# Kernel tuning notes

Measured on AMD Instinct MI355X. Metric: run time of the kernel, lower is better.

Reference implementation:

```python
import jax, jax.numpy as jnp
import numpy as np

B, T, P, D = 32, 8, 196, 768
M = 10
NUM_CLASSES = 100
NUM_IDX = 98
P_MASK = 0.5


def setup_inputs() -> dict:
    key = jax.random.key(0)
    ks = jax.random.split(key, 16)
    s = 0.02
    inp = {
        'visual': jax.random.normal(ks[0], (B, T * P, D), jnp.float32),
        'audio': jax.random.normal(ks[1], (B, D), jnp.float32),
        'causal': jax.random.normal(ks[2], (B, M, D), jnp.float32),
        'random_mask': jax.random.uniform(ks[3], (B, T, P, D)) < P_MASK,
        'Wa': jax.random.normal(ks[4], (D, D), jnp.float32) * s,
        'ba': jnp.zeros((D,), jnp.float32),
        'Wv': jax.random.normal(ks[5], (D, D), jnp.float32) * s,
        'bv': jnp.zeros((D,), jnp.float32),
        'Waa': jax.random.normal(ks[6], (D, D), jnp.float32) * s,
        'baa': jnp.zeros((D,), jnp.float32),
        'Wav': jax.random.normal(ks[7], (D, D), jnp.float32) * s,
        'bav': jnp.zeros((D,), jnp.float32),
        'Wf': jax.random.normal(ks[8], (D, D), jnp.float32) * s,
        'bf': jnp.zeros((D,), jnp.float32),
        'Wf2': jax.random.normal(ks[9], (D, 1), jnp.float32) * s,
        'bf2': jnp.zeros((1,), jnp.float32),
        'Wc': jax.random.normal(ks[10], (D, NUM_CLASSES), jnp.float32) * s,
        'bc': jnp.zeros((NUM_CLASSES,), jnp.float32),
        'causal_param': jnp.zeros((1,), jnp.float32),
    }
    return inp


def reference(visual, audio, causal, random_mask, Wa, ba, Wv, bv, Waa, baa,
              Wav, bav, Wf, bf, Wf2, bf2, Wc, bc, causal_param):
    vis = visual.reshape(visual.shape[0], T, -1, D)  # [B,8,196,768]

    # causal_intervention_mean_feature4
    cp = jax.nn.sigmoid(causal_param)                 # soft_clamp2, [1]
    feats = causal @ Wf + bf                          # [B,M,D]
    feats2 = jnp.swapaxes(causal @ Wf2 + bf2, 1, 2)   # [B,1,M]
    fw = jax.nn.softmax(jnp.tanh(feats), axis=1)      # [B,M,D]
    ci = jnp.einsum('bom,bmd->bd', feats2, fw * causal)  # bmm + squeeze
    audio2 = cp * ci + audio                          # [B,D]

    # audio_visual_attention1
    pa = jnp.tanh(audio2 @ Waa + baa)                 # [B,D]
    pv = jnp.tanh(vis @ Wav + bav)                    # [B,T,P,D]
    sscore = pv * pa[:, None, None, :]                # einsum ijkd,id->ijkd
    sattn = jax.nn.softmax(sscore, axis=2)            # softmax over patches
    patch = jnp.sum(sattn, axis=-1)                   # [B,T,P]
    thresh = jnp.sort(patch, axis=-1)[:, :, NUM_IDX]  # per (b,t) threshold
    spa_mask = patch < thresh[:, :, None]             # [B,T,P]
    final_mask = ~(spa_mask[..., None] & random_mask) # [B,T,P,D]
    sfilt = jnp.where(final_mask, sattn, 0.0)

    sav = jnp.sum(sfilt * pv, axis=2)                 # [B,T,D]
    tattn = jax.nn.softmax(sav * pa[:, None, :], axis=1)

    vp = jnp.sum(sfilt * vis, axis=2)                 # [B,T,D]
    vp = jnp.sum(tattn * vp, axis=1)                  # [B,D]

    af = jax.nn.relu(audio2 @ Wa + ba)
    vf = jax.nn.relu(vp @ Wv + bv)
    logits = (af + vf) @ Wc + bc                      # [B,num_classes]
    return logits
```

## Files before the change

kernel.cpp:

```cpp
#include <hip/hip_runtime.h>
#include <hip/hip_bf16.h>
#include <hip/hip_fp16.h>
#include <math.h>

#define BB 32
#define TT 8
#define PP 196
#define DD 768
#define MM 10
#define NCLS 100
#define NIDX 98

typedef __attribute__((ext_vector_type(8))) short short8v;
typedef __attribute__((ext_vector_type(4))) float float4v;

__device__ __forceinline__ float fast_tanh(float x) {
    float e = __expf(2.0f * x);
    return 1.0f - 2.0f / (e + 1.0f);
}
__device__ __forceinline__ unsigned short f2bf(float x) {
    __hip_bfloat16 h = __float2bfloat16(x);
    return *(unsigned short*)&h;
}
__device__ __forceinline__ float bf2f(unsigned short h) {
    return __uint_as_float(((unsigned)h) << 16);
}
__device__ __forceinline__ unsigned short f2h(float x) {
    __half h = __float2half(x);
    return *(unsigned short*)&h;
}
__device__ __forceinline__ float h2f(unsigned short u) {
    __half h = *(__half*)&u;
    return __half2float(h);
}

__global__ __launch_bounds__(256) void k_prep(
    const float* __restrict__ vis, unsigned short* __restrict__ visb,
    const unsigned int* __restrict__ rm, int* __restrict__ mode) {
    const size_t NC = (size_t)BB * TT * PP * DD / 8;
    size_t gid = (size_t)blockIdx.x * 256 + threadIdx.x;
    size_t nthr = (size_t)gridDim.x * 256;
    for (size_t i = gid; i < NC; i += nthr) {
        const float4* s = (const float4*)(vis + i * 8);
        float4 x = s[0], y = s[1];
        __hip_bfloat162 h;
        unsigned int u0, u1, u2, u3;
        h = __float22bfloat162_rn(make_float2(x.x, x.y)); u0 = *(unsigned int*)&h;
        h = __float22bfloat162_rn(make_float2(x.z, x.w)); u1 = *(unsigned int*)&h;
        h = __float22bfloat162_rn(make_float2(y.x, y.y)); u2 = *(unsigned int*)&h;
        h = __float22bfloat162_rn(make_float2(y.z, y.w)); u3 = *(unsigned int*)&h;
        uint4 o; o.x = u0; o.y = u1; o.z = u2; o.w = u3;
        ((uint4*)visb)[i] = o;
    }
    if (blockIdx.x == 0) {
        __shared__ int f_ni, f_nf;
        if (threadIdx.x == 0) { f_ni = 0; f_nf = 0; }
        __syncthreads();
        int ni = 0, nf = 0;
        for (int i = threadIdx.x; i < 16384; i += 256) {
            unsigned int v = rm[i];
            ni |= (v > 1u) ? 1 : 0;
            nf |= (v != 0u && v != 0x3F800000u) ? 1 : 0;
        }
        if (ni) atomicOr(&f_ni, 1);
        if (nf) atomicOr(&f_nf, 1);
        __syncthreads();
        if (threadIdx.x == 0) *mode = f_ni ? (f_nf ? 2 : 1) : 0;
    }
}

__global__ __launch_bounds__(256) void k_split_w(const float* __restrict__ W,
    unsigned short* __restrict__ ht) {
    __shared__ float tile[32][33];
    int bn = blockIdx.x * 32;
    int bk = blockIdx.y * 32;
    int tx = threadIdx.x & 31, ty = threadIdx.x >> 5;
    #pragma unroll
    for (int i = 0; i < 4; ++i)
        tile[ty + i * 8][tx] = W[(size_t)(bk + ty + i * 8) * DD + bn + tx];
    __syncthreads();
    #pragma unroll
    for (int i = 0; i < 4; ++i) {
        int n = bn + ty + i * 8, k = bk + tx;
        ht[(size_t)n * DD + k] = f2bf(tile[tx][ty + i * 8]);
    }
}

__global__ __launch_bounds__(768) void k_feats_partial(
    const float* __restrict__ causal, const float* __restrict__ Wf,
    const float* __restrict__ Wf2,
    float* __restrict__ pf, float* __restrict__ pf2) {
    int b = blockIdx.x, kc = blockIdx.y;
    int k0 = kc * 256;
    int t = threadIdx.x;
    __shared__ float cs[MM][256];
    __shared__ float red[MM][12];
    for (int i = t; i < MM * 256; i += 768)
        cs[i >> 8][i & 255] = causal[((size_t)b * MM + (i >> 8)) * DD + k0 + (i & 255)];
    __syncthreads();
    int wave = t >> 6, lane = t & 63;
    float w2v = (t < 256) ? Wf2[k0 + t] : 0.f;
    #pragma unroll
    for (int m = 0; m < MM; ++m) {
        float p = (t < 256) ? cs[m][t] * w2v : 0.f;
        #pragma unroll
        for (int o = 32; o > 0; o >>= 1) p += __shfl_down(p, o);
        if (lane == 0) red[m][wave] = p;
    }
    __syncthreads();
    if (t < MM) {
        float s = 0.f;
        #pragma unroll
        for (int wv = 0; wv < 4; ++wv) s += red[t][wv];
        pf2[(b * 3 + kc) * MM + t] = s;
    }
    float acc[MM];
    #pragma unroll
    for (int m = 0; m < MM; ++m) acc[m] = 0.f;
    #pragma unroll 4
    for (int k = 0; k < 256; ++k) {
        float wv = Wf[(size_t)(k0 + k) * DD + t];
        #pragma unroll
        for (int m = 0; m < MM; ++m) acc[m] = fmaf(cs[m][k], wv, acc[m]);
    }
    #pragma unroll
    for (int m = 0; m < MM; ++m)
        pf[(((size_t)b * 3 + kc) * MM + m) * DD + t] = acc[m];
}

__global__ __launch_bounds__(768) void k_audio2a(
    const float* __restrict__ causal, const float* __restrict__ audio,
    const float* __restrict__ pf, const float* __restrict__ pf2,
    const float* __restrict__ bf, const float* __restrict__ bf2,
    const float* __restrict__ cparam, float* __restrict__ a2) {
    int b = blockIdx.x;
    int t = threadIdx.x;
    float cp = 1.0f / (1.0f + __expf(-cparam[0]));
    float tf[MM], f2[MM];
    float mx = -1e30f;
    #pragma unroll
    for (int m = 0; m < MM; ++m) {
        float acc = bf[t];
        float s2 = bf2[0];
        #pragma unroll
        for (int kc = 0; kc < 3; ++kc) {
            acc += pf[(((size_t)b * 3 + kc) * MM + m) * DD + t];
            s2 += pf2[(b * 3 + kc) * MM + m];
        }
        tf[m] = fast_tanh(acc);
        f2[m] = s2;
        mx = fmaxf(mx, tf[m]);
    }
    float s = 0.f;
    #pragma unroll
    for (int m = 0; m < MM; ++m) { tf[m] = __expf(tf[m] - mx); s += tf[m]; }
    float inv = 1.0f / s;
    float ci = 0.f;
    #pragma unroll
    for (int m = 0; m < MM; ++m)
        ci += f2[m] * (tf[m] * inv) * causal[((size_t)b * MM + m) * DD + t];
    a2[(size_t)b * DD + t] = cp * ci + audio[(size_t)b * DD + t];
}

__global__ __launch_bounds__(256) void k_audio2b(
    const float* __restrict__ a2,
    const float* __restrict__ Waa, const float* __restrict__ baa,
    const float* __restrict__ Wa, const float* __restrict__ ba,
    float* __restrict__ pa, float* __restrict__ af, float* __restrict__ colsum) {
    int gid0 = (blockIdx.y * 24 + blockIdx.x) * 256 + threadIdx.x;
    for (int i = gid0; i < BB * TT * DD; i += 48 * 256) colsum[i] = 0.f;
    __shared__ float a2s[16][DD + 4];
    int sel = blockIdx.y;
    const float* W = sel ? Wa : Waa;
    int t = threadIdx.x;
    int c = blockIdx.x * 32 + (t & 31);
    int slot = t >> 5;
    float bias = sel ? ba[c] : baa[c];
    #pragma unroll
    for (int g = 0; g < 2; ++g) {
        if (g) __syncthreads();
        for (int i = t; i < 16 * DD; i += 256)
            a2s[i / DD][i % DD] = a2[(size_t)(g * 16 + i / DD) * DD + i % DD];
        __syncthreads();
        float acc0 = 0.f, acc1 = 0.f;
        #pragma unroll 8
        for (int k = 0; k < DD; ++k) {
            float wv = W[(size_t)k * DD + c];
            acc0 = fmaf(a2s[slot][k], wv, acc0);
            acc1 = fmaf(a2s[slot + 8][k], wv, acc1);
        }
        int b0 = g * 16 + slot, b1 = b0 + 8;
        if (sel == 0) {
            pa[(size_t)b0 * DD + c] = fast_tanh(acc0 + bias);
            pa[(size_t)b1 * DD + c] = fast_tanh(acc1 + bias);
        } else {
            af[(size_t)b0 * DD + c] = fmaxf(acc0 + bias, 0.f);
            af[(size_t)b1 * DD + c] = fmaxf(acc1 + bias, 0.f);
        }
    }
}

__global__ __launch_bounds__(256, 5) void k_pv_mfma(
    const unsigned short* __restrict__ visb, const unsigned short* __restrict__ Wht,
    const float* __restrict__ bav, const float* __restrict__ pa,
    unsigned short* __restrict__ pvh, float* __restrict__ colsum)
{
    __shared__ unsigned short As[128 * 64];
    __shared__ unsigned short Bs[128 * 64];
    int wg = blockIdx.x;
    int lin = (wg & 7) * 294 + (wg >> 3);
    int mt = lin / 6, nt = lin % 6;
    int i0 = mt * 128, n0 = nt * 128;
    int t = threadIdx.x, w = t >> 6, l = t & 63;
    int wm = (w >> 1) * 64, wn = (w & 1) * 64;

    float4v zero4 = {0.f, 0.f, 0.f, 0.f};
    float4v acc[4][4];
    #pragma unroll
    for (int a = 0; a < 4; ++a)
        #pragma unroll
        for (int b = 0; b < 4; ++b) acc[a][b] = zero4;

    int brow[4], bcs[4];
    #pragma unroll
    for (int j = 0; j < 4; ++j) {
        int row = (w * 4 + j) * 8 + (l >> 3);
        brow[j] = row;
        bcs[j] = (l & 7) ^ (row & 7);
    }

    for (int wnd = 0; wnd < 12; ++wnd) {
        __syncthreads();
        int kw = wnd * 64;
        #pragma unroll
        for (int j = 0; j < 4; ++j) {
            size_t aoff = (size_t)(i0 + brow[j]) * DD + kw + bcs[j] * 8;
            __builtin_amdgcn_global_load_lds(
                (const __attribute__((address_space(1))) unsigned int*)(visb + aoff),
                (__attribute__((address_space(3))) unsigned int*)&As[(w * 4 + j) * 512],
                16, 0, 0);
            size_t boff = (size_t)(n0 + brow[j]) * DD + kw + bcs[j] * 8;
            __builtin_amdgcn_global_load_lds(
                (const __attribute__((address_space(1))) unsigned int*)(Wht + boff),
                (__attribute__((address_space(3))) unsigned int*)&Bs[(w * 4 + j) * 512],
                16, 0, 0);
        }
        __syncthreads();
        #pragma unroll
        for (int kk = 0; kk < 2; ++kk) {
            short8v ahf[4], bhf[4];
            #pragma unroll
            for (int mr = 0; mr < 4; ++mr) {
                int row = wm + mr * 16 + (l & 15);
                int c = kk * 4 + (l >> 4);
                ahf[mr] = *(const short8v*)&As[row * 64 + ((c ^ (row & 7)) * 8)];
            }
            #pragma unroll
            for (int nc = 0; nc < 4; ++nc) {
                int row = wn + nc * 16 + (l & 15);
                int c = kk * 4 + (l >> 4);
                bhf[nc] = *(const short8v*)&Bs[row * 64 + ((c ^ (row & 7)) * 8)];
            }
            #pragma unroll
            for (int mr = 0; mr < 4; ++mr)
                #pragma unroll
                for (int nc = 0; nc < 4; ++nc)
                    acc[mr][nc] = __builtin_amdgcn_mfma_f32_16x16x32_bf16(
                        ahf[mr], bhf[nc], acc[mr][nc], 0, 0, 0);
        }
    }
    float* cred = (float*)&As[0];
    __syncthreads();
    if (t < 256) cred[t] = 0.f;
    __syncthreads();
    int bt0 = i0 / PP;
    int btbound = (bt0 + 1) * PP;
    #pragma unroll
    for (int nc = 0; nc < 4; ++nc) {
        int cl = wn + nc * 16 + (l & 15);
        int col = n0 + cl;
        float bias = bav[col];
        #pragma unroll
        for (int mr = 0; mr < 4; ++mr) {
            int row0 = i0 + wm + mr * 16 + ((l >> 4) << 2);
            int bq = row0 / (TT * PP);
            float pav = pa[(size_t)bq * DD + col];
            float esum = 0.f;
            #pragma unroll
            for (int v = 0; v < 4; ++v) {
                unsigned short pb = f2h(fast_tanh(acc[mr][nc][v] + bias));
                pvh[(size_t)(row0 + v) * DD + col] = pb;
                esum += __expf(h2f(pb) * pav);
            }
            int btg = (row0 >= btbound) ? 1 : 0;
            atomicAdd(&cred[btg * 128 + cl], esum);
        }
    }
    __syncthreads();
    if (t < 256) {
        int btg = t >> 7, cl = t & 127;
        if (btg == 0 || btbound < i0 + 128)
            atomicAdd(&colsum[(size_t)(bt0 + btg) * DD + n0 + cl], cred[t]);
    }
}

__global__ __launch_bounds__(768) void k_patch(
    const unsigned short* __restrict__ pvh, const float* __restrict__ pa,
    const float* __restrict__ colsum, unsigned char* __restrict__ spa_g) {
    int bt = blockIdx.x;
    int b = bt >> 3;
    size_t base = (size_t)bt * PP * DD;
    __shared__ float2 pi[DD];
    __shared__ float patch[PP];
    int t = threadIdx.x;
    float pav = pa[(size_t)b * DD + t];
    float inv = 1.0f / colsum[(size_t)bt * DD + t];
    pi[t] = make_float2(pav, inv);
    __syncthreads();
    int wave = t >> 6, lane = t & 63;
    for (int p = wave; p < PP; p += 12) {
        const uint2* rv = (const uint2*)(pvh + base + (size_t)p * DD);
        float sum = 0.f;
        #pragma unroll
        for (int j = lane; j < 192; j += 64) {
            uint2 v = rv[j];
            int c = j * 4;
            float2 q0 = pi[c], q1 = pi[c + 1], q2 = pi[c + 2], q3 = pi[c + 3];
            sum += __expf(h2f((unsigned short)(v.x & 0xFFFFu)) * q0.x) * q0.y
                 + __expf(h2f((unsigned short)(v.x >> 16)) * q1.x) * q1.y
                 + __expf(h2f((unsigned short)(v.y & 0xFFFFu)) * q2.x) * q2.y
                 + __expf(h2f((unsigned short)(v.y >> 16)) * q3.x) * q3.y;
        }
        #pragma unroll
        for (int o = 32; o > 0; o >>= 1) sum += __shfl_down(sum, o);
        if (lane == 0) patch[p] = sum;
    }
    __syncthreads();
    if (t < PP) {
        float x = patch[t];
        int c = 0;
        for (int q = 0; q < PP; ++q) c += (patch[q] <= x) ? 1 : 0;
        spa_g[bt * PP + t] = (c <= NIDX) ? 1 : 0;
    }
}

__global__ __launch_bounds__(768) void k_masked(
    const unsigned short* __restrict__ pvh, const unsigned short* __restrict__ visb,
    const void* __restrict__ rmask, const int* __restrict__ mode_p,
    const float* __restrict__ pa, const float* __restrict__ colsum,
    const unsigned char* __restrict__ spa_g,
    float* __restrict__ sav, float* __restrict__ vpt) {
    int bt = blockIdx.x;
    int half = blockIdx.y;
    int b = bt >> 3;
    size_t base = (size_t)bt * PP * DD;
    __shared__ unsigned char spa[PP];
    __shared__ float red_s[2][384];
    __shared__ float red_v[2][384];
    int t = threadIdx.x;
    if (t < PP) spa[t] = spa_g[bt * PP + t];
    int pg = (t >= 384) ? 1 : 0;
    int c = t - pg * 384;
    int col = half * 384 + c;
    int p0 = pg * 98, p1 = p0 + 98;
    float pav = pa[(size_t)b * DD + col];
    float inv = 1.0f / colsum[(size_t)bt * DD + col];
    __syncthreads();
    const unsigned short* pvb = pvh + base + col;
    const unsigned short* vib = visb + base + col;
    float sava = 0.f, vpa = 0.f;
    int mode = *mode_p;
    if (mode == 0) {
        const int* mb = (const int*)rmask + base + col;
        #pragma unroll 7
        for (int p = p0; p < p1; ++p) {
            float pvv = h2f(pvb[(size_t)p * DD]);
            float sa = __expf(pvv * pav) * inv;
            bool km = !(spa[p] && (mb[(size_t)p * DD] != 0));
            if (km) { sava = fmaf(sa, pvv, sava); vpa = fmaf(sa, bf2f(vib[(size_t)p * DD]), vpa); }
        }
    } else if (mode == 1) {
        const float* mb = (const float*)rmask + base + col;
        #pragma unroll 7
        for (int p = p0; p < p1; ++p) {
            float pvv = h2f(pvb[(size_t)p * DD]);
            float sa = __expf(pvv * pav) * inv;
            bool km = !(spa[p] && (mb[(size_t)p * DD] != 0.f));
            if (km) { sava = fmaf(sa, pvv, sava); vpa = fmaf(sa, bf2f(vib[(size_t)p * DD]), vpa); }
        }
    } else {
        const unsigned char* mb = (const unsigned char*)rmask + base + col;
        #pragma unroll 7
        for (int p = p0; p < p1; ++p) {
            float pvv = h2f(pvb[(size_t)p * DD]);
            float sa = __expf(pvv * pav) * inv;
            bool km = !(spa[p] && (mb[(size_t)p * DD] != 0));
            if (km) { sava = fmaf(sa, pvv, sava); vpa = fmaf(sa, bf2f(vib[(size_t)p * DD]), vpa); }
        }
    }
    red_s[pg][c] = sava;
    red_v[pg][c] = vpa;
    __syncthreads();
    if (t < 384) {
        int col2 = half * 384 + t;
        sav[(size_t)bt * DD + col2] = red_s[0][t] + red_s[1][t];
        vpt[(size_t)bt * DD + col2] = red_v[0][t] + red_v[1][t];
    }
}

__global__ __launch_bounds__(768) void k_tail_a(
    const float* __restrict__ sav, const float* __restrict__ vpt,
    const float* __restrict__ pa, float* __restrict__ vp) {
    int b = blockIdx.x;
    int t = threadIdx.x;
    float pav = pa[(size_t)b * DD + t];
    float x[TT];
    float mx = -1e30f;
    #pragma unroll
    for (int k = 0; k < TT; ++k) {
        x[k] = sav[((size_t)b * TT + k) * DD + t] * pav;
        mx = fmaxf(mx, x[k]);
    }
    float s = 0.f;
    #pragma unroll
    for (int k = 0; k < TT; ++k) { x[k] = __expf(x[k] - mx); s += x[k]; }
    float inv = 1.0f / s;
    float acc = 0.f;
    #pragma unroll
    for (int k = 0; k < TT; ++k)
        acc += x[k] * inv * vpt[((size_t)b * TT + k) * DD + t];
    vp[(size_t)b * DD + t] = acc;
}

__global__ __launch_bounds__(256) void k_tail_b(
    const float* __restrict__ vp, const float* __restrict__ af,
    const float* __restrict__ Wv, const float* __restrict__ bv,
    float* __restrict__ h) {
    __shared__ float vs[16][DD + 4];
    int t = threadIdx.x;
    int c = blockIdx.x * 32 + (t & 31);
    int slot = t >> 5;
    float bias = bv[c];
    #pragma unroll
    for (int g = 0; g < 2; ++g) {
        if (g) __syncthreads();
        for (int i = t; i < 16 * DD; i += 256)
            vs[i / DD][i % DD] = vp[(size_t)(g * 16 + i / DD) * DD + i % DD];
        __syncthreads();
        float acc0 = 0.f, acc1 = 0.f;
        #pragma unroll 8
        for (int k = 0; k < DD; ++k) {
            float wv = Wv[(size_t)k * DD + c];
            acc0 = fmaf(vs[slot][k], wv, acc0);
            acc1 = fmaf(vs[slot + 8][k], wv, acc1);
        }
        int b0 = g * 16 + slot, b1 = b0 + 8;
        h[(size_t)b0 * DD + c] = fmaxf(acc0 + bias, 0.f) + af[(size_t)b0 * DD + c];
        h[(size_t)b1 * DD + c] = fmaxf(acc1 + bias, 0.f) + af[(size_t)b1 * DD + c];
    }
}

__global__ __launch_bounds__(256) void k_tail_c(
    const float* __restrict__ h, const float* __restrict__ Wc,
    const float* __restrict__ bc, float* __restrict__ out) {
    int t = threadIdx.x;
    int c = blockIdx.x * 8 + (t & 7);
    int b = t >> 3;
    if (c >= NCLS) return;
    float acc = bc[c];
    #pragma unroll 8
    for (int k = 0; k < DD; ++k)
        acc = fmaf(h[(size_t)b * DD + k], Wc[(size_t)k * NCLS + c], acc);
    out[(size_t)b * NCLS + c] = acc;
}

extern "C" void kernel_launch(void* const* d_in, const int* in_sizes, int n_in,
                              void* d_out, int out_size, void* d_ws, size_t ws_size,
                              hipStream_t stream) {
    const float* visual = (const float*)d_in[0];
    const float* audio  = (const float*)d_in[1];
    const float* causal = (const float*)d_in[2];
    const void*  rmask  = d_in[3];
    const float* Wa   = (const float*)d_in[4];
    const float* ba   = (const float*)d_in[5];
    const float* Wv   = (const float*)d_in[6];
    const float* bv   = (const float*)d_in[7];
    const float* Waa  = (const float*)d_in[8];
    const float* baa  = (const float*)d_in[9];
    const float* Wav  = (const float*)d_in[10];
    const float* bav  = (const float*)d_in[11];
    const float* Wf   = (const float*)d_in[12];
    const float* bf   = (const float*)d_in[13];
    const float* Wf2  = (const float*)d_in[14];
    const float* bf2  = (const float*)d_in[15];
    const float* Wc   = (const float*)d_in[16];
    const float* bc   = (const float*)d_in[17];
    const float* cpar = (const float*)d_in[18];
    float* out = (float*)d_out;

    const size_t NE = (size_t)BB * TT * PP * DD;
    unsigned short* Wht = (unsigned short*)d_ws;
    float* pfreg = (float*)(Wht + (size_t)DD * DD);
    float* colsum = pfreg;
    float* savw  = colsum + (size_t)BB * TT * DD;
    float* vptw  = savw + (size_t)BB * TT * DD;
    float* vpw   = vptw + (size_t)BB * TT * DD;
    float* hw    = vpw + (size_t)BB * DD;
    unsigned char* spa_g = (unsigned char*)(hw + (size_t)BB * DD);
    float* pf    = pfreg;
    float* pf2   = pfreg + (size_t)BB * 3 * MM * DD;
    float* a2w   = pf2 + 1024;
    float* paw   = a2w + (size_t)BB * DD;
    float* afw   = paw + (size_t)BB * DD;
    int*   modew = (int*)(afw + (size_t)BB * DD);
    unsigned short* visb = (unsigned short*)(modew + 16);
    unsigned short* pvh  = visb + NE;

    k_prep<<<2048, 256, 0, stream>>>(visual, visb, (const unsigned int*)rmask, modew);
    k_split_w<<<dim3(24, 24), 256, 0, stream>>>(Wav, Wht);
    k_feats_partial<<<dim3(BB, 3), 768, 0, stream>>>(causal, Wf, Wf2, pf, pf2);
    k_audio2a<<<BB, 768, 0, stream>>>(causal, audio, pf, pf2, bf, bf2, cpar, a2w);
    k_audio2b<<<dim3(24, 2), 256, 0, stream>>>(a2w, Waa, baa, Wa, ba, paw, afw, colsum);
    k_pv_mfma<<<2352, 256, 0, stream>>>(visb, Wht, bav, paw, pvh, colsum);
    k_patch<<<BB * TT, 768, 0, stream>>>(pvh, paw, colsum, spa_g);
    k_masked<<<dim3(BB * TT, 2), 768, 0, stream>>>(pvh, visb, rmask, modew, paw,
                                                   colsum, spa_g, savw, vptw);
    k_tail_a<<<BB, 768, 0, stream>>>(savw, vptw, paw, vpw);
    k_tail_b<<<24, 256, 0, stream>>>(vpw, afw, Wv, bv, hw);
    k_tail_c<<<13, 256, 0, stream>>>(hw, Wc, bc, out);
}
```

Baseline: 532.7 us.

## Merge prep kernels, double-buffer GEMM LDS, and stage pv output through LDS

Folds the bf16 conversion, weight transpose and feats-partial kernels into one launch that dispatches on block index, removing two kernel launches. The pv MFMA GEMM now double-buffers its A/B tiles in LDS so the next K-window's global->LDS loads overlap the current MFMAs, with one barrier per iteration. The fp16 pv tile is first written to swizzled LDS and then stored to global memory as coalesced 16-byte rows. The price is twice the LDS per block, which lowers the occupancy hint from 5 to 2 blocks per CU and may hurt latency hiding.

```diff
diff --git a/kernel.cpp b/kernel.cpp
--- a/kernel.cpp
+++ b/kernel.cpp
@@ -34,98 +34,103 @@
     return __half2float(h);
 }
 
-__global__ __launch_bounds__(256) void k_prep(
+__global__ __launch_bounds__(768) void k_prep_all(
     const float* __restrict__ vis, unsigned short* __restrict__ visb,
-    const unsigned int* __restrict__ rm, int* __restrict__ mode) {
-    const size_t NC = (size_t)BB * TT * PP * DD / 8;
-    size_t gid = (size_t)blockIdx.x * 256 + threadIdx.x;
-    size_t nthr = (size_t)gridDim.x * 256;
-    for (size_t i = gid; i < NC; i += nthr) {
-        const float4* s = (const float4*)(vis + i * 8);
-        float4 x = s[0], y = s[1];
-        __hip_bfloat162 h;
-        unsigned int u0, u1, u2, u3;
-        h = __float22bfloat162_rn(make_float2(x.x, x.y)); u0 = *(unsigned int*)&h;
-        h = __float22bfloat162_rn(make_float2(x.z, x.w)); u1 = *(unsigned int*)&h;
-        h = __float22bfloat162_rn(make_float2(y.x, y.y)); u2 = *(unsigned int*)&h;
-        h = __float22bfloat162_rn(make_float2(y.z, y.w)); u3 = *(unsigned int*)&h;
-        uint4 o; o.x = u0; o.y = u1; o.z = u2; o.w = u3;
-        ((uint4*)visb)[i] = o;
-    }
-    if (blockIdx.x == 0) {
-        __shared__ int f_ni, f_nf;
-        if (threadIdx.x == 0) { f_ni = 0; f_nf = 0; }
-        __syncthreads();
-        int ni = 0, nf = 0;
-        for (int i = threadIdx.x; i < 16384; i += 256) {
-            unsigned int v = rm[i];
-            ni |= (v > 1u) ? 1 : 0;
-            nf |= (v != 0u && v != 0x3F800000u) ? 1 : 0;
-        }
-        if (ni) atomicOr(&f_ni, 1);
-        if (nf) atomicOr(&f_nf, 1);
-        __syncthreads();
-        if (threadIdx.x == 0) *mode = f_ni ? (f_nf ? 2 : 1) : 0;
-    }
-}
-
-__global__ __launch_bounds__(256) void k_split_w(const float* __restrict__ W,
-    unsigned short* __restrict__ ht) {
-    __shared__ float tile[32][33];
-    int bn = blockIdx.x * 32;
-    int bk = blockIdx.y * 32;
-    int tx = threadIdx.x & 31, ty = threadIdx.x >> 5;
-    #pragma unroll
-    for (int i = 0; i < 4; ++i)
-        tile[ty + i * 8][tx] = W[(size_t)(bk + ty + i * 8) * DD + bn + tx];
-    __syncthreads();
-    #pragma unroll
-    for (int i = 0; i < 4; ++i) {
-        int n = bn + ty + i * 8, k = bk + tx;
-        ht[(size_t)n * DD + k] = f2bf(tile[tx][ty + i * 8]);
-    }
-}
-
-__global__ __launch_bounds__(768) void k_feats_partial(
+    const unsigned int* __restrict__ rm, int* __restrict__ mode,
+    const float* __restrict__ Wav, unsigned short* __restrict__ Wht,
     const float* __restrict__ causal, const float* __restrict__ Wf,
     const float* __restrict__ Wf2,
     float* __restrict__ pf, float* __restrict__ pf2) {
-    int b = blockIdx.x, kc = blockIdx.y;
-    int k0 = kc * 256;
-    int t = threadIdx.x;
-    __shared__ float cs[MM][256];
-    __shared__ float red[MM][12];
-    for (int i = t; i < MM * 256; i += 768)
-        cs[i >> 8][i & 255] = causal[((size_t)b * MM + (i >> 8)) * DD + k0 + (i & 255)];
-    __syncthreads();
-    int wave = t >> 6, lane = t & 63;
-    float w2v = (t < 256) ? Wf2[k0 + t] : 0.f;
-    #pragma unroll
-    for (int m = 0; m < MM; ++m) {
-        float p = (t < 256) ? cs[m][t] * w2v : 0.f;
-        #pragma unroll
-        for (int o = 32; o > 0; o >>= 1) p += __shfl_down(p, o);
-        if (lane == 0) red[m][wave] = p;
-    }
-    __syncthreads();
-    if (t < MM) {
-        float s = 0.f;
-        #pragma unroll
-        for (int wv = 0; wv < 4; ++wv) s += red[t][wv];
-        pf2[(b * 3 + kc) * MM + t] = s;
-    }
-    float acc[MM];
-    #pragma unroll
-    for (int m = 0; m < MM; ++m) acc[m] = 0.f;
-    #pragma unroll 4
-    for (int k = 0; k < 256; ++k) {
-        float wv = Wf[(size_t)(k0 + k) * DD + t];
-        #pragma unroll
-        for (int m = 0; m < MM; ++m) acc[m] = fmaf(cs[m][k], wv, acc[m]);
-    }
-    #pragma unroll
-    for (int m = 0; m < MM; ++m)
-        pf[(((size_t)b * 3 + kc) * MM + m) * DD + t] = acc[m];
+    int t = threadIdx.x;
+    int bid = blockIdx.x;
+    if (bid < 1024) {
+        const size_t NC = (size_t)BB * TT * PP * DD / 8;
+        size_t gid = (size_t)bid * 768 + t;
+        for (size_t i = gid; i < NC; i += 1024 * 768) {
+            const float4* s = (const float4*)(vis + i * 8);
+            float4 x = s[0], y = s[1];
+            __hip_bfloat162 h;
+            unsigned int u0, u1, u2, u3;
+            h = __float22bfloat162_rn(make_float2(x.x, x.y)); u0 = *(unsigned int*)&h;
+            h = __float22bfloat162_rn(make_float2(x.z, x.w)); u1 = *(unsigned int*)&h;
+            h = __float22bfloat162_rn(make_float2(y.x, y.y)); u2 = *(unsigned int*)&h;
+            h = __float22bfloat162_rn(make_float2(y.z, y.w)); u3 = *(unsigned int*)&h;
+            uint4 o; o.x = u0; o.y = u1; o.z = u2; o.w = u3;
+            ((uint4*)visb)[i] = o;
+        }
+        if (bid == 0) {
+            __shared__ int f_ni, f_nf;
+            if (t == 0) { f_ni = 0; f_nf = 0; }
+            __syncthreads();
+            int ni = 0, nf = 0;
+            for (int i = t; i < 16384; i += 768) {
+                unsigned int v = rm[i];
+                ni |= (v > 1u) ? 1 : 0;
+                nf |= (v != 0u && v != 0x3F800000u) ? 1 : 0;
+            }
+            if (ni) atomicOr(&f_ni, 1);
+            if (nf) atomicOr(&f_nf, 1);
+            __syncthreads();
+            if (t == 0) *mode = f_ni ? (f_nf ? 2 : 1) : 0;
+        }
+    } else if (bid < 1600) {
+        __shared__ float tile[32][33];
+        int bb = bid - 1024;
+        int bn = (bb % 24) * 32;
+        int bk = (bb / 24) * 32;
+        if (t < 256) {
+            int tx = t & 31, ty = t >> 5;
+            #pragma unroll
+            for (int i = 0; i < 4; ++i)
+                tile[ty + i * 8][tx] = Wav[(size_t)(bk + ty + i * 8) * DD + bn + tx];
+        }
+        __syncthreads();
+        if (t < 256) {
+            int tx = t & 31, ty = t >> 5;
+            #pragma unroll
+            for (int i = 0; i < 4; ++i) {
+                int n = bn + ty + i * 8, k = bk + tx;
+                Wht[(size_t)n * DD + k] = f2bf(tile[tx][ty + i * 8]);
+            }
+        }
+    } else {
+        __shared__ float cs[MM][256];
+        __shared__ float red[MM][12];
+        int bb = bid - 1600;
+        int b = bb % 32, kc = bb / 32;
+        int k0 = kc * 256;
+        for (int i = t; i < MM * 256; i += 768)
+            cs[i >> 8][i & 255] = causal[((size_t)b * MM + (i >> 8)) * DD + k0 + (i & 255)];
+        __syncthreads();
+        int wave = t >> 6, lane = t & 63;
+        float w2v = (t < 256) ? Wf2[k0 + t] : 0.f;
+        #pragma unroll
+        for (int m = 0; m < MM; ++m) {
+            float p = (t < 256) ? cs[m][t] * w2v : 0.f;
+            #pragma unroll
+            for (int o = 32; o > 0; o >>= 1) p += __shfl_down(p, o);
+            if (lane == 0) red[m][wave] = p;
+        }
+        __syncthreads();
+        if (t < MM) {
+            float s = 0.f;
+            #pragma unroll
+            for (int wv = 0; wv < 4; ++wv) s += red[t][wv];
+            pf2[(b * 3 + kc) * MM + t] = s;
+        }
+        float acc[MM];
+        #pragma unroll
+        for (int m = 0; m < MM; ++m) acc[m] = 0.f;
+        #pragma unroll 4
+        for (int k = 0; k < 256; ++k) {
+            float wv = Wf[(size_t)(k0 + k) * DD + t];
+            #pragma unroll
+            for (int m = 0; m < MM; ++m) acc[m] = fmaf(cs[m][k], wv, acc[m]);
+        }
+        #pragma unroll
+        for (int m = 0; m < MM; ++m)
+            pf[(((size_t)b * 3 + kc) * MM + m) * DD + t] = acc[m];
+    }
 }
 
 __global__ __launch_bounds__(768) void k_audio2a(
@@ -200,13 +205,13 @@
     }
 }
 
-__global__ __launch_bounds__(256, 5) void k_pv_mfma(
+__global__ __launch_bounds__(256, 2) void k_pv_mfma(
     const unsigned short* __restrict__ visb, const unsigned short* __restrict__ Wht,
     const float* __restrict__ bav, const float* __restrict__ pa,
     unsigned short* __restrict__ pvh, float* __restrict__ colsum)
 {
-    __shared__ unsigned short As[128 * 64];
-    __shared__ unsigned short Bs[128 * 64];
+    __shared__ unsigned short As[2][128 * 64];
+    __shared__ unsigned short Bs[2][128 * 64];
     int wg = blockIdx.x;
     int lin = (wg & 7) * 294 + (wg >> 3);
     int mt = lin / 6, nt = lin % 6;
@@ -229,23 +234,29 @@
         bcs[j] = (l & 7) ^ (row & 7);
     }
 
+#define STAGE(bb, wnd_)                                                          \
+    {                                                                            \
+        int kw_ = (wnd_) * 64;                                                   \
+        _Pragma("unroll")                                                        \
+        for (int j = 0; j < 4; ++j) {                                            \
+            size_t aoff_ = (size_t)(i0 + brow[j]) * DD + kw_ + bcs[j] * 8;       \
+            __builtin_amdgcn_global_load_lds(                                    \
+                (const __attribute__((address_space(1))) unsigned int*)(visb + aoff_), \
+                (__attribute__((address_space(3))) unsigned int*)&As[bb][(w * 4 + j) * 512], \
+                16, 0, 0);                                                       \
+            size_t boff_ = (size_t)(n0 + brow[j]) * DD + kw_ + bcs[j] * 8;       \
+            __builtin_amdgcn_global_load_lds(                                    \
+                (const __attribute__((address_space(1))) unsigned int*)(Wht + boff_), \
+                (__attribute__((address_space(3))) unsigned int*)&Bs[bb][(w * 4 + j) * 512], \
+                16, 0, 0);                                                       \
+        }                                                                        \
+    }
+
+    STAGE(0, 0);
+    __syncthreads();
     for (int wnd = 0; wnd < 12; ++wnd) {
-        __syncthreads();
-        int kw = wnd * 64;
-        #pragma unroll
-        for (int j = 0; j < 4; ++j) {
-            size_t aoff = (size_t)(i0 + brow[j]) * DD + kw + bcs[j] * 8;
-            __builtin_amdgcn_global_load_lds(
-                (const __attribute__((address_space(1))) unsigned int*)(visb + aoff),
-                (__attribute__((address_space(3))) unsigned int*)&As[(w * 4 + j) * 512],
-                16, 0, 0);
-            size_t boff = (size_t)(n0 + brow[j]) * DD + kw + bcs[j] * 8;
-            __builtin_amdgcn_global_load_lds(
-                (const __attribute__((address_space(1))) unsigned int*)(Wht + boff),
-                (__attribute__((address_space(3))) unsigned int*)&Bs[(w * 4 + j) * 512],
-                16, 0, 0);
-        }
-        __syncthreads();
+        int cur = wnd & 1;
+        if (wnd < 11) STAGE(cur ^ 1, wnd + 1);
         #pragma unroll
         for (int kk = 0; kk < 2; ++kk) {
             short8v ahf[4], bhf[4];
@@ -253,13 +264,13 @@
             for (int mr = 0; mr < 4; ++mr) {
                 int row = wm + mr * 16 + (l & 15);
                 int c = kk * 4 + (l >> 4);
-                ahf[mr] = *(const short8v*)&As[row * 64 + ((c ^ (row & 7)) * 8)];
+                ahf[mr] = *(const short8v*)&As[cur][row * 64 + ((c ^ (row & 7)) * 8)];
             }
             #pragma unroll
             for (int nc = 0; nc < 4; ++nc) {
                 int row = wn + nc * 16 + (l & 15);
                 int c = kk * 4 + (l >> 4);
-                bhf[nc] = *(const short8v*)&Bs[row * 64 + ((c ^ (row & 7)) * 8)];
+                bhf[nc] = *(const short8v*)&Bs[cur][row * 64 + ((c ^ (row & 7)) * 8)];
             }
             #pragma unroll
             for (int mr = 0; mr < 4; ++mr)
@@ -268,9 +279,11 @@
                     acc[mr][nc] = __builtin_amdgcn_mfma_f32_16x16x32_bf16(
                         ahf[mr], bhf[nc], acc[mr][nc], 0, 0, 0);
         }
-    }
-    float* cred = (float*)&As[0];
-    __syncthreads();
+        __syncthreads();
+    }
+#undef STAGE
+    unsigned short* Cl = &As[0][0];
+    float* cred = (float*)&Bs[0][0];
     if (t < 256) cred[t] = 0.f;
     __syncthreads();
     int bt0 = i0 / PP;
@@ -282,14 +295,17 @@
         float bias = bav[col];
         #pragma unroll
         for (int mr = 0; mr < 4; ++mr) {
-            int row0 = i0 + wm + mr * 16 + ((l >> 4) << 2);
+            int lr0 = wm + mr * 16 + ((l >> 4) << 2);
+            int row0 = i0 + lr0;
             int bq = row0 / (TT * PP);
             float pav = pa[(size_t)bq * DD + col];
             float esum = 0.f;
             #pragma unroll
             for (int v = 0; v < 4; ++v) {
                 unsigned short pb = f2h(fast_tanh(acc[mr][nc][v] + bias));
-                pvh[(size_t)(row0 + v) * DD + col] = pb;
+                int lr = lr0 + v;
+                int boff = lr * 256 + ((cl * 2) ^ ((lr & 7) << 4));
+                *(unsigned short*)((char*)Cl + boff) = pb;
                 esum += __expf(h2f(pb) * pav);
             }
             int btg = (row0 >= btbound) ? 1 : 0;
@@ -297,6 +313,18 @@
         }
     }
     __syncthreads();
+    #pragma unroll
+    for (int rb = 0; rb < 2; ++rb) {
+        int lr = (t >> 2) + rb * 64;
+        size_t grow = (size_t)(i0 + lr) * DD + n0;
+        #pragma unroll
+        for (int q = 0; q < 4; ++q) {
+            int ch = (t & 3) + q * 4;
+            int boff = lr * 256 + ((ch * 16) ^ ((lr & 7) << 4));
+            uint4 val = *(uint4*)((char*)Cl + boff);
+            *(uint4*)(pvh + grow + ch * 8) = val;
+        }
+    }
     if (t < 256) {
         int btg = t >> 7, cl = t & 127;
         if (btg == 0 || btbound < i0 + 128)
@@ -516,9 +544,8 @@
     unsigned short* visb = (unsigned short*)(modew + 16);
     unsigned short* pvh  = visb + NE;
 
-    k_prep<<<2048, 256, 0, stream>>>(visual, visb, (const unsigned int*)rmask, modew);
-    k_split_w<<<dim3(24, 24), 256, 0, stream>>>(Wav, Wht);
-    k_feats_partial<<<dim3(BB, 3), 768, 0, stream>>>(causal, Wf, Wf2, pf, pf2);
+    k_prep_all<<<1696, 768, 0, stream>>>(visual, visb, (const unsigned int*)rmask,
+                                         modew, Wav, Wht, causal, Wf, Wf2, pf, pf2);
     k_audio2a<<<BB, 768, 0, stream>>>(causal, audio, pf, pf2, bf, bf2, cpar, a2w);
     k_audio2b<<<dim3(24, 2), 256, 0, stream>>>(a2w, Waa, baa, Wa, ba, paw, afw, colsum);
     k_pv_mfma<<<2352, 256, 0, stream>>>(visb, Wht, bav, paw, pvh, colsum);
```

Measured after the change: 505.6 us. -5.1%, faster.
